# Kernel tuning notes

Measured on AMD Instinct MI355X. Metric: run time of the kernel, lower is better.

Reference implementation:

```python
import jax, jax.numpy as jnp
import numpy as np

N_HEADS = 4

def log_cosh(x):
    # numerically stable log(cosh(x)) = |x| + log1p(exp(-2|x|)) - log(2)
    ax = jnp.abs(x)
    return ax + jnp.log1p(jnp.exp(-2.0 * ax)) - jnp.log(2.0)

def setup_inputs() -> dict:
    key = jax.random.key(0)
    ks = jax.random.split(key, 7)
    B, I, A, E, H = 4, 2048, 2048, 256, N_HEADS
    return {
        "query": jax.random.normal(ks[0], (B, I, E), dtype=jnp.float32),
        "key": jax.random.normal(ks[1], (B, A, E), dtype=jnp.float32),
        "value": jax.random.normal(ks[2], (B, A, E), dtype=jnp.float32),
        "distances": jax.random.uniform(ks[3], (B, I, A), dtype=jnp.float32),
        "in_proj_w": jax.random.normal(ks[4], (3 * E, E), dtype=jnp.float32) * 0.05,
        "out_proj_w": jax.random.normal(ks[5], (E, E), dtype=jnp.float32) * 0.05,
        "mass_w": jax.random.normal(ks[6], (H, E), dtype=jnp.float32) * 0.05,
    }

def reference(query, key, value, distances, in_proj_w, out_proj_w, mass_w):
    B, I, E = query.shape
    A = key.shape[1]
    H = N_HEADS
    D = E // H
    # distance-decay additive bias: mass is (B, A, H), nonnegative via log_cosh
    mass = log_cosh(key @ mass_w.T)                       # (B, A, H)
    bias = jnp.einsum('bah,bia->bhia', -mass, distances)  # (B, H, I, A)
    # nn.MultiheadAttention (bias=False) projections
    wq, wk, wv = jnp.split(in_proj_w, 3, axis=0)          # each (E, E)
    q = (query @ wq.T).reshape(B, I, H, D).transpose(0, 2, 1, 3)  # (B,H,I,D)
    k = (key @ wk.T).reshape(B, A, H, D).transpose(0, 2, 1, 3)    # (B,H,A,D)
    v = (value @ wv.T).reshape(B, A, H, D).transpose(0, 2, 1, 3)  # (B,H,A,D)
    scale = 1.0 / jnp.sqrt(jnp.asarray(D, dtype=q.dtype))
    scores = jnp.einsum('bhid,bhad->bhia', q, k) * scale + bias
    attn = jax.nn.softmax(scores, axis=-1)
    o = jnp.einsum('bhia,bhad->bhid', attn, v)            # (B,H,I,D)
    o = o.transpose(0, 2, 1, 3).reshape(B, I, E)
    return o @ out_proj_w.T
```

## Files before the change

kernel.cpp:

```cpp
#include <hip/hip_runtime.h>
#include <hip/hip_bf16.h>
#include <math.h>

#define BB 4
#define II 2048
#define AA 2048
#define EE 256
#define HH 4

#define LOG2E 1.4426950408889634f
#define SCL   (0.125f * LOG2E)

typedef __bf16 bf16_t;
typedef bf16_t bf16x8 __attribute__((ext_vector_type(8)));
typedef bf16_t bf16x4 __attribute__((ext_vector_type(4)));
typedef float  f32x4  __attribute__((ext_vector_type(4)));

static __device__ __forceinline__ f32x4 mfma16(bf16x8 a, bf16x8 b, f32x4 c) {
    return __builtin_amdgcn_mfma_f32_16x16x32_bf16(a, b, c, 0, 0, 0);
}

static __device__ __forceinline__ void glds16(const bf16_t* g, const bf16_t* l) {
    __builtin_amdgcn_global_load_lds(
        (const __attribute__((address_space(1))) void*)g,
        (__attribute__((address_space(3))) void*)l, 16, 0, 0);
}

static __device__ __forceinline__ void proj_body(
    const float* __restrict__ Aop, const float* __restrict__ Bop,
    bf16_t* __restrict__ Cout, int m0, int n0, int TRANS, float cscale,
    bf16_t (*sA)[72], bf16_t (*sB)[72])
{
    const int t = threadIdx.x;
    const int w = t >> 6, l = t & 63, g = l >> 4, q = l & 15;
    const int wm = w >> 1, wn = w & 1;
    const int r = t >> 2, s = t & 3;

    f32x4 acc[2][2] = {};

    for (int kt = 0; kt < 4; ++kt) {
        {
            const float* ga = Aop + (size_t)(m0 + r) * EE + kt * 64 + s * 16;
            float tmp[16];
            *(f32x4*)&tmp[0]  = *(const f32x4*)(ga + 0);
            *(f32x4*)&tmp[4]  = *(const f32x4*)(ga + 4);
            *(f32x4*)&tmp[8]  = *(const f32x4*)(ga + 8);
            *(f32x4*)&tmp[12] = *(const f32x4*)(ga + 12);
            bf16x8 w0, w1;
            #pragma unroll
            for (int i = 0; i < 8; ++i) { w0[i] = (bf16_t)tmp[i]; w1[i] = (bf16_t)tmp[8 + i]; }
            *(bf16x8*)&sA[r][s * 16]     = w0;
            *(bf16x8*)&sA[r][s * 16 + 8] = w1;
        }
        {
            const float* gb = Bop + (size_t)(n0 + r) * EE + kt * 64 + s * 16;
            float tmp[16];
            *(f32x4*)&tmp[0]  = *(const f32x4*)(gb + 0);
            *(f32x4*)&tmp[4]  = *(const f32x4*)(gb + 4);
            *(f32x4*)&tmp[8]  = *(const f32x4*)(gb + 8);
            *(f32x4*)&tmp[12] = *(const f32x4*)(gb + 12);
            bf16x8 w0, w1;
            #pragma unroll
            for (int i = 0; i < 8; ++i) { w0[i] = (bf16_t)tmp[i]; w1[i] = (bf16_t)tmp[8 + i]; }
            *(bf16x8*)&sB[r][s * 16]     = w0;
            *(bf16x8*)&sB[r][s * 16 + 8] = w1;
        }
        __syncthreads();
        #pragma unroll
        for (int ks = 0; ks < 2; ++ks) {
            bf16x8 aA[2], aB[2];
            #pragma unroll
            for (int f = 0; f < 2; ++f) {
                aA[f] = *(const bf16x8*)&sA[wm * 32 + f * 16 + q][ks * 32 + g * 8];
                aB[f] = *(const bf16x8*)&sB[wn * 32 + f * 16 + q][ks * 32 + g * 8];
            }
            #pragma unroll
            for (int fm = 0; fm < 2; ++fm)
            #pragma unroll
            for (int fn = 0; fn < 2; ++fn)
                acc[fm][fn] = mfma16(aA[fm], aB[fn], acc[fm][fn]);
        }
        __syncthreads();
    }
    #pragma unroll
    for (int fm = 0; fm < 2; ++fm)
    #pragma unroll
    for (int fn = 0; fn < 2; ++fn)
    #pragma unroll
    for (int j = 0; j < 4; ++j) {
        const int m = m0 + wm * 32 + fm * 16 + g * 4 + j;
        const int n = n0 + wn * 32 + fn * 16 + q;
        const bf16_t v = (bf16_t)(acc[fm][fn][j] * cscale);
        if (TRANS == 0) {
            Cout[(size_t)m * EE + n] = v;
        } else {
            const int bb = n >> 11, a = n & (AA - 1);
            const int a6 = a & 63;
            const int p6 = (a6 & 32) | ((a6 & 12) << 1) | ((a6 & 16) >> 2) | (a6 & 3);
            Cout[(size_t)bb * (AA * EE) + (size_t)(a >> 6) * (EE * 64) + m * 64 + p6] = v;
        }
    }
}

__global__ __launch_bounds__(256) void fused_pre(
    const float* __restrict__ query, const float* __restrict__ key,
    const float* __restrict__ value, const float* __restrict__ in_w,
    const float* __restrict__ mass_w,
    bf16_t* __restrict__ Qp, bf16_t* __restrict__ Kp, bf16_t* __restrict__ Vt,
    float* __restrict__ massT)
{
    __shared__ __align__(16) bf16_t sA[64][72];
    __shared__ __align__(16) bf16_t sB[64][72];
    const int z = blockIdx.z;
    if (z == 0) {
        proj_body(query, in_w, Qp, blockIdx.x * 64, blockIdx.y * 64, 0, SCL, sA, sB);
    } else if (z == 1) {
        proj_body(key, in_w + 65536, Kp, blockIdx.x * 64, blockIdx.y * 64, 0, 1.0f, sA, sB);
    } else if (z == 2) {
        proj_body(in_w + 131072, value, Vt, blockIdx.y * 64, blockIdx.x * 64, 1, 1.0f, sA, sB);
    } else {
        const int w = threadIdx.x >> 6, l = threadIdx.x & 63;
        const int p = blockIdx.y * 128 + blockIdx.x;
        const int row0 = p * 16 + w * 4;
        f32x4 mw[HH];
        #pragma unroll
        for (int hh = 0; hh < HH; ++hh)
            mw[hh] = *(const f32x4*)(mass_w + hh * EE + l * 4);
        #pragma unroll
        for (int rr = 0; rr < 4; ++rr) {
            const int row = row0 + rr;
            f32x4 kv = *(const f32x4*)(key + (size_t)row * EE + l * 4);
            f32x4 sd;
            #pragma unroll
            for (int hh = 0; hh < HH; ++hh)
                sd[hh] = kv[0]*mw[hh][0] + kv[1]*mw[hh][1] + kv[2]*mw[hh][2] + kv[3]*mw[hh][3];
            #pragma unroll
            for (int off = 32; off >= 1; off >>= 1) {
                #pragma unroll
                for (int hh = 0; hh < HH; ++hh) sd[hh] += __shfl_xor(sd[hh], off, 64);
            }
            if (l == 0) {
                const int bb = row >> 11, a = row & (AA - 1);
                #pragma unroll
                for (int hh = 0; hh < HH; ++hh) {
                    float ax = fabsf(sd[hh]);
                    massT[((size_t)bb * HH + hh) * AA + a] =
                        (ax + log1pf(__expf(-2.0f * ax)) - 0.693147180559945f) * LOG2E;
                }
            }
        }
    }
}

__global__ __launch_bounds__(256) void out_gemm(
    const bf16_t* __restrict__ Aop, const float* __restrict__ Bop,
    float* __restrict__ Cout)
{
    __shared__ __align__(16) bf16_t sA[64][72];
    __shared__ __align__(16) bf16_t sB[64][72];
    const int t = threadIdx.x;
    const int w = t >> 6, l = t & 63, g = l >> 4, q = l & 15;
    const int wm = w >> 1, wn = w & 1;
    const int m0 = blockIdx.x * 64, n0 = blockIdx.y * 64;
    const int r = t >> 2, s = t & 3;

    f32x4 acc[2][2] = {};

    for (int kt = 0; kt < 4; ++kt) {
        {
            const bf16_t* ga = Aop + (size_t)(m0 + r) * EE + kt * 64 + s * 16;
            *(bf16x8*)&sA[r][s * 16]     = *(const bf16x8*)(ga);
            *(bf16x8*)&sA[r][s * 16 + 8] = *(const bf16x8*)(ga + 8);
        }
        {
            const float* gb = Bop + (size_t)(n0 + r) * EE + kt * 64 + s * 16;
            float tmp[16];
            *(f32x4*)&tmp[0]  = *(const f32x4*)(gb + 0);
            *(f32x4*)&tmp[4]  = *(const f32x4*)(gb + 4);
            *(f32x4*)&tmp[8]  = *(const f32x4*)(gb + 8);
            *(f32x4*)&tmp[12] = *(const f32x4*)(gb + 12);
            bf16x8 w0, w1;
            #pragma unroll
            for (int i = 0; i < 8; ++i) { w0[i] = (bf16_t)tmp[i]; w1[i] = (bf16_t)tmp[8 + i]; }
            *(bf16x8*)&sB[r][s * 16]     = w0;
            *(bf16x8*)&sB[r][s * 16 + 8] = w1;
        }
        __syncthreads();
        #pragma unroll
        for (int ks = 0; ks < 2; ++ks) {
            bf16x8 aA[2], aB[2];
            #pragma unroll
            for (int f = 0; f < 2; ++f) {
                aA[f] = *(const bf16x8*)&sA[wm * 32 + f * 16 + q][ks * 32 + g * 8];
                aB[f] = *(const bf16x8*)&sB[wn * 32 + f * 16 + q][ks * 32 + g * 8];
            }
            #pragma unroll
            for (int fm = 0; fm < 2; ++fm)
            #pragma unroll
            for (int fn = 0; fn < 2; ++fn)
                acc[fm][fn] = mfma16(aA[fm], aB[fn], acc[fm][fn]);
        }
        __syncthreads();
    }
    #pragma unroll
    for (int fm = 0; fm < 2; ++fm)
    #pragma unroll
    for (int fn = 0; fn < 2; ++fn)
    #pragma unroll
    for (int j = 0; j < 4; ++j) {
        const int m = m0 + wm * 32 + fm * 16 + g * 4 + j;
        const int n = n0 + wn * 32 + fn * 16 + q;
        Cout[(size_t)m * EE + n] = acc[fm][fn][j];
    }
}

__global__ __launch_bounds__(512, 4) void attn_kernel(
    const bf16_t* __restrict__ Qp, const bf16_t* __restrict__ Kp,
    const bf16_t* __restrict__ Vt, const float* __restrict__ massT,
    const float* __restrict__ dist, bf16_t* __restrict__ Obuf)
{
    __shared__ __align__(16) bf16_t sK[2][2][4096];
    __shared__ __align__(16) bf16_t sV[2][2][4096];
    __shared__ __align__(16) float  sM[2048];

    const int t = threadIdx.x;
    const int wv = t >> 6, l = t & 63, g = l >> 4, q = l & 15;
    const int s = wv >> 2, rg = wv & 3;
    const int h = blockIdx.y, b = blockIdx.z;
    const int i0 = blockIdx.x * 64;

    *(f32x4*)&sM[t * 4] = *(const f32x4*)(massT + ((size_t)b * HH + h) * AA + t * 4);

    bf16x8 qf[2];
    #pragma unroll
    for (int ks = 0; ks < 2; ++ks)
        qf[ks] = *(const bf16x8*)(Qp + (size_t)(b * II + i0 + rg * 16 + q) * EE
                                     + h * 64 + ks * 32 + g * 8);

    const int u0 = rg * 2;
    const int drow0 = u0 * 8 + (l >> 3);
    const int cs = (l & 7) ^ (drow0 & 7);

    const bf16_t* pkg = Kp + ((size_t)b * AA + s * 64 + drow0) * EE + h * 64 + cs * 8;
    const bf16_t* pvg = Vt + (size_t)b * (AA * EE) + (size_t)s * (EE * 64)
                           + (size_t)(h * 64 + drow0) * 64 + cs * 8;
    const float*  pdg = dist + ((size_t)b * II + i0 + rg * 16 + q) * AA + s * 64 + g * 4;

    auto stage = [&](int kb) {
        #pragma unroll
        for (int u = 0; u < 2; ++u) {
            glds16(pkg + u * (8 * EE), &sK[s][kb][(u0 + u) * 512]);
            glds16(pvg + u * (8 * 64), &sV[s][kb][(u0 + u) * 512]);
        }
    };

    f32x4 rd[4];
    auto load_dist = [&]() {
        #pragma unroll
        for (int fa = 0; fa < 4; ++fa) rd[fa] = *(const f32x4*)(pdg + fa * 16);
    };

    stage(0);
    pkg += 128 * EE; pvg += 2 * (EE * 64);
    load_dist();
    pdg += 128;
    __syncthreads();

    float mrun = -INFINITY;
    f32x4 oacc[4] = {};
    f32x4 lacc = {};
    bf16x8 vone;
    #pragma unroll
    for (int j = 0; j < 8; ++j) vone[j] = (bf16_t)1.0f;

    int ma = s * 64;

    #pragma unroll 2
    for (int k = 0; k < 16; ++k) {
        const int kb = k & 1;
        if (k < 15) {
            stage(kb ^ 1);
            pkg += 128 * EE; pvg += 2 * (EE * 64);
        }

        f32x4 st[4] = {};
        __builtin_amdgcn_s_setprio(1);
        #pragma unroll
        for (int fa = 0; fa < 4; ++fa) {
            const int row = fa * 16 + q;
            #pragma unroll
            for (int ks = 0; ks < 2; ++ks) {
                bf16x8 ak = *(const bf16x8*)&sK[s][kb][row * 64 + (((ks * 4 + g) ^ (row & 7)) * 8)];
                st[fa] = mfma16(ak, qf[ks], st[fa]);
            }
        }
        __builtin_amdgcn_s_setprio(0);

        float mloc = -INFINITY;
        #pragma unroll
        for (int fa = 0; fa < 4; ++fa) {
            f32x4 ms = *(const f32x4*)&sM[ma + fa * 16 + g * 4];
            #pragma unroll
            for (int j = 0; j < 4; ++j) {
                float sv = fmaf(-ms[j], rd[fa][j], st[fa][j]);
                st[fa][j] = sv;
                mloc = fmaxf(mloc, sv);
            }
        }
        ma += 128;
        if (k < 15) { load_dist(); pdg += 128; }

        mloc = fmaxf(mloc, __shfl_xor(mloc, 16, 64));
        mloc = fmaxf(mloc, __shfl_xor(mloc, 32, 64));
        const bool skip = __all(mloc <= mrun + 8.0f);
        float mnew = mrun;
        if (!skip) {
            mnew = fmaxf(mrun, mloc);
            const float sc = exp2f(mrun - mnew);
            mrun = mnew;
            float osc[4];
            #pragma unroll
            for (int j = 0; j < 4; ++j) osc[j] = __shfl(sc, g * 4 + j, 64);
            #pragma unroll
            for (int fd = 0; fd < 4; ++fd)
            #pragma unroll
            for (int j = 0; j < 4; ++j) oacc[fd][j] *= osc[j];
            #pragma unroll
            for (int j = 0; j < 4; ++j) lacc[j] *= osc[j];
        }

        #pragma unroll
        for (int fa = 0; fa < 4; ++fa)
        #pragma unroll
        for (int j = 0; j < 4; ++j)
            st[fa][j] = exp2f(st[fa][j] - mnew);

        bf16x8 pa[2];
        #pragma unroll
        for (int ka = 0; ka < 2; ++ka)
        #pragma unroll
        for (int j = 0; j < 8; ++j)
            pa[ka][j] = (bf16_t)st[2 * ka + (j >> 2)][j & 3];

        __builtin_amdgcn_s_setprio(1);
        #pragma unroll
        for (int ka = 0; ka < 2; ++ka) {
            #pragma unroll
            for (int fd = 0; fd < 4; ++fd) {
                const int row = fd * 16 + q;
                bf16x8 bv = *(const bf16x8*)&sV[s][kb][row * 64 + (((ka * 4 + g) ^ (row & 7)) * 8)];
                oacc[fd] = mfma16(pa[ka], bv, oacc[fd]);
            }
            lacc = mfma16(pa[ka], vone, lacc);
        }
        __builtin_amdgcn_s_setprio(0);

        __syncthreads();
    }

    float* cb = (float*)&sK[0][0][0];
    if (s == 1) {
        float* p = cb + (rg * 64 + l) * 24;
        p[0] = mrun;
        *(f32x4*)(p + 4) = lacc;
        #pragma unroll
        for (int fd = 0; fd < 4; ++fd) *(f32x4*)(p + 8 + fd * 4) = oacc[fd];
    }
    __syncthreads();
    if (s == 0) {
        const float* p = cb + (rg * 64 + l) * 24;
        const float mB = p[0];
        const f32x4 lB = *(const f32x4*)(p + 4);
        const float mS = fmaxf(mrun, mB);
        const float aS = exp2f(mrun - mS), bS = exp2f(mB - mS);
        float aSo[4], bSo[4], inv[4];
        #pragma unroll
        for (int j = 0; j < 4; ++j) {
            aSo[j] = __shfl(aS, g * 4 + j, 64);
            bSo[j] = __shfl(bS, g * 4 + j, 64);
        }
        #pragma unroll
        for (int j = 0; j < 4; ++j)
            inv[j] = 1.0f / (lacc[j] * aSo[j] + lB[j] * bSo[j]);
        #pragma unroll
        for (int fd = 0; fd < 4; ++fd) {
            f32x4 ob = *(const f32x4*)(p + 8 + fd * 4);
            #pragma unroll
            for (int j = 0; j < 4; ++j) {
                const float o = (oacc[fd][j] * aSo[j] + ob[j] * bSo[j]) * inv[j];
                Obuf[(size_t)(b * II + i0 + rg * 16 + g * 4 + j) * EE
                     + h * 64 + fd * 16 + q] = (bf16_t)o;
            }
        }
    }
}

extern "C" void kernel_launch(void* const* d_in, const int* in_sizes, int n_in,
                              void* d_out, int out_size, void* d_ws, size_t ws_size,
                              hipStream_t stream)
{
    const float* query  = (const float*)d_in[0];
    const float* key    = (const float*)d_in[1];
    const float* value  = (const float*)d_in[2];
    const float* dist   = (const float*)d_in[3];
    const float* in_w   = (const float*)d_in[4];
    const float* out_w  = (const float*)d_in[5];
    const float* mass_w = (const float*)d_in[6];
    float* out = (float*)d_out;

    char* ws = (char*)d_ws;
    bf16_t* Qp    = (bf16_t*)(ws);
    bf16_t* Kp    = (bf16_t*)(ws + 1 * 4194304);
    bf16_t* Vt    = (bf16_t*)(ws + 2 * 4194304);
    bf16_t* Obuf  = (bf16_t*)(ws + 3 * 4194304);
    float*  massT = (float*) (ws + 4 * 4194304);

    fused_pre<<<dim3(128, 4, 4), dim3(256), 0, stream>>>(
        query, key, value, in_w, mass_w, Qp, Kp, Vt, massT);
    attn_kernel<<<dim3(32, 4, 4), dim3(512), 0, stream>>>(Qp, Kp, Vt, massT, dist, Obuf);
    out_gemm<<<dim3(128, 4), dim3(256), 0, stream>>>(Obuf, out_w, out);
}
```

Before: 81.59 us.

## Restructure attention into 16-row blocks with 4-way key split reading K/V directly

The attention kernel now gives each block 16 query rows and splits the key axis four ways across waves. K, V and mass are loaded straight from global memory into registers rather than staged through LDS with barriers. The grid becomes 1D with an XCD-aware mapping so blocks sharing a batch and head land on the same XCD, improving L2 reuse. This removes LDS staging and per-iteration syncs, but adds repeated global reads of K/V across many more blocks and a 4-way merge at the end.

New measurement: 213.4 us. +161.6%, slower.

```diff
diff --git a/kernel.cpp b/kernel.cpp
--- a/kernel.cpp
+++ b/kernel.cpp
@@ -18,12 +18,6 @@
 
 static __device__ __forceinline__ f32x4 mfma16(bf16x8 a, bf16x8 b, f32x4 c) {
     return __builtin_amdgcn_mfma_f32_16x16x32_bf16(a, b, c, 0, 0, 0);
-}
-
-static __device__ __forceinline__ void glds16(const bf16_t* g, const bf16_t* l) {
-    __builtin_amdgcn_global_load_lds(
-        (const __attribute__((address_space(1))) void*)g,
-        (__attribute__((address_space(3))) void*)l, 16, 0, 0);
 }
 
 static __device__ __forceinline__ void proj_body(
@@ -214,57 +208,42 @@
     }
 }
 
-__global__ __launch_bounds__(512, 4) void attn_kernel(
+__global__ __launch_bounds__(256, 4) void attn_kernel(
     const bf16_t* __restrict__ Qp, const bf16_t* __restrict__ Kp,
     const bf16_t* __restrict__ Vt, const float* __restrict__ massT,
     const float* __restrict__ dist, bf16_t* __restrict__ Obuf)
 {
-    __shared__ __align__(16) bf16_t sK[2][2][4096];
-    __shared__ __align__(16) bf16_t sV[2][2][4096];
-    __shared__ __align__(16) float  sM[2048];
-
-    const int t = threadIdx.x;
-    const int wv = t >> 6, l = t & 63, g = l >> 4, q = l & 15;
-    const int s = wv >> 2, rg = wv & 3;
-    const int h = blockIdx.y, b = blockIdx.z;
-    const int i0 = blockIdx.x * 64;
-
-    *(f32x4*)&sM[t * 4] = *(const f32x4*)(massT + ((size_t)b * HH + h) * AA + t * 4);
+    __shared__ __align__(16) float cmb[3][64][25];
+
+    const int t0 = threadIdx.x;
+    const int w = t0 >> 6, l = t0 & 63, g = l >> 4, q = l & 15;
+
+    const int lin = blockIdx.x;
+    const int xcd = lin & 7;
+    const int r   = lin >> 3;
+    const int bh  = xcd * 2 + (r >> 7);
+    const int it  = r & 127;
+    const int b = bh >> 2, h = bh & 3;
+    const int i0 = it * 16;
 
     bf16x8 qf[2];
     #pragma unroll
     for (int ks = 0; ks < 2; ++ks)
-        qf[ks] = *(const bf16x8*)(Qp + (size_t)(b * II + i0 + rg * 16 + q) * EE
-                                     + h * 64 + ks * 32 + g * 8);
-
-    const int u0 = rg * 2;
-    const int drow0 = u0 * 8 + (l >> 3);
-    const int cs = (l & 7) ^ (drow0 & 7);
-
-    const bf16_t* pkg = Kp + ((size_t)b * AA + s * 64 + drow0) * EE + h * 64 + cs * 8;
-    const bf16_t* pvg = Vt + (size_t)b * (AA * EE) + (size_t)s * (EE * 64)
-                           + (size_t)(h * 64 + drow0) * 64 + cs * 8;
-    const float*  pdg = dist + ((size_t)b * II + i0 + rg * 16 + q) * AA + s * 64 + g * 4;
-
-    auto stage = [&](int kb) {
-        #pragma unroll
-        for (int u = 0; u < 2; ++u) {
-            glds16(pkg + u * (8 * EE), &sK[s][kb][(u0 + u) * 512]);
-            glds16(pvg + u * (8 * 64), &sV[s][kb][(u0 + u) * 512]);
-        }
-    };
-
-    f32x4 rd[4];
-    auto load_dist = [&]() {
-        #pragma unroll
-        for (int fa = 0; fa < 4; ++fa) rd[fa] = *(const f32x4*)(pdg + fa * 16);
-    };
-
-    stage(0);
-    pkg += 128 * EE; pvg += 2 * (EE * 64);
-    load_dist();
-    pdg += 128;
-    __syncthreads();
+        qf[ks] = *(const bf16x8*)(Qp + (size_t)(b * II + i0 + q) * EE + h * 64 + ks * 32 + g * 8);
+
+    const bf16_t* pK[4];
+    #pragma unroll
+    for (int fa = 0; fa < 4; ++fa)
+        pK[fa] = Kp + ((size_t)b * AA + w * 64 + fa * 16 + q) * EE + h * 64 + g * 8;
+    const bf16_t* pV = Vt + (size_t)b * (AA * EE) + (size_t)w * (EE * 64)
+                          + (h * 64 + q) * 64 + g * 8;
+    const float* pM = massT + ((size_t)b * HH + h) * AA + w * 64 + g * 4;
+    const float* pD = dist + (size_t)(b * II + i0 + q) * AA + w * 64 + g * 4;
+
+    f32x4 rd[2][4];
+    #pragma unroll
+    for (int fa = 0; fa < 4; ++fa) rd[0][fa] = *(const f32x4*)(pD + fa * 16);
+    pD += 256;
 
     float mrun = -INFINITY;
     f32x4 oacc[4] = {};
@@ -273,42 +252,54 @@
     #pragma unroll
     for (int j = 0; j < 8; ++j) vone[j] = (bf16_t)1.0f;
 
-    int ma = s * 64;
-
     #pragma unroll 2
-    for (int k = 0; k < 16; ++k) {
-        const int kb = k & 1;
-        if (k < 15) {
-            stage(kb ^ 1);
-            pkg += 128 * EE; pvg += 2 * (EE * 64);
+    for (int t = 0; t < 8; ++t) {
+        bf16x8 ak[4][2];
+        #pragma unroll
+        for (int fa = 0; fa < 4; ++fa)
+        #pragma unroll
+        for (int ks = 0; ks < 2; ++ks)
+            ak[fa][ks] = *(const bf16x8*)(pK[fa] + ks * 32);
+
+        if (t < 7) {
+            #pragma unroll
+            for (int fa = 0; fa < 4; ++fa)
+                rd[(t + 1) & 1][fa] = *(const f32x4*)(pD + fa * 16);
+            pD += 256;
         }
 
         f32x4 st[4] = {};
         __builtin_amdgcn_s_setprio(1);
         #pragma unroll
+        for (int fa = 0; fa < 4; ++fa)
+        #pragma unroll
+        for (int ks = 0; ks < 2; ++ks)
+            st[fa] = mfma16(ak[fa][ks], qf[ks], st[fa]);
+        __builtin_amdgcn_s_setprio(0);
+
+        bf16x8 vv[2][4];
+        #pragma unroll
+        for (int ka = 0; ka < 2; ++ka)
+        #pragma unroll
+        for (int fd = 0; fd < 4; ++fd)
+            vv[ka][fd] = *(const bf16x8*)(pV + fd * (16 * 64) + ka * 32);
+
+        float mloc = -INFINITY;
+        #pragma unroll
         for (int fa = 0; fa < 4; ++fa) {
-            const int row = fa * 16 + q;
-            #pragma unroll
-            for (int ks = 0; ks < 2; ++ks) {
-                bf16x8 ak = *(const bf16x8*)&sK[s][kb][row * 64 + (((ks * 4 + g) ^ (row & 7)) * 8)];
-                st[fa] = mfma16(ak, qf[ks], st[fa]);
-            }
-        }
-        __builtin_amdgcn_s_setprio(0);
-
-        float mloc = -INFINITY;
-        #pragma unroll
-        for (int fa = 0; fa < 4; ++fa) {
-            f32x4 ms = *(const f32x4*)&sM[ma + fa * 16 + g * 4];
+            f32x4 ms = *(const f32x4*)(pM + fa * 16);
             #pragma unroll
             for (int j = 0; j < 4; ++j) {
-                float sv = fmaf(-ms[j], rd[fa][j], st[fa][j]);
+                float sv = fmaf(-ms[j], rd[t & 1][fa][j], st[fa][j]);
                 st[fa][j] = sv;
                 mloc = fmaxf(mloc, sv);
             }
         }
-        ma += 128;
-        if (k < 15) { load_dist(); pdg += 128; }
+
+        #pragma unroll
+        for (int fa = 0; fa < 4; ++fa) pK[fa] += 256 * EE;
+        pV += 4 * (EE * 64);
+        pM += 256;
 
         mloc = fmaxf(mloc, __shfl_xor(mloc, 16, 64));
         mloc = fmaxf(mloc, __shfl_xor(mloc, 32, 64));
@@ -346,51 +337,54 @@
         #pragma unroll
         for (int ka = 0; ka < 2; ++ka) {
             #pragma unroll
-            for (int fd = 0; fd < 4; ++fd) {
-                const int row = fd * 16 + q;
-                bf16x8 bv = *(const bf16x8*)&sV[s][kb][row * 64 + (((ka * 4 + g) ^ (row & 7)) * 8)];
-                oacc[fd] = mfma16(pa[ka], bv, oacc[fd]);
-            }
+            for (int fd = 0; fd < 4; ++fd)
+                oacc[fd] = mfma16(pa[ka], vv[ka][fd], oacc[fd]);
             lacc = mfma16(pa[ka], vone, lacc);
         }
         __builtin_amdgcn_s_setprio(0);
-
-        __syncthreads();
-    }
-
-    float* cb = (float*)&sK[0][0][0];
-    if (s == 1) {
-        float* p = cb + (rg * 64 + l) * 24;
+    }
+
+    if (w > 0) {
+        float* p = &cmb[w - 1][l][0];
         p[0] = mrun;
         *(f32x4*)(p + 4) = lacc;
         #pragma unroll
         for (int fd = 0; fd < 4; ++fd) *(f32x4*)(p + 8 + fd * 4) = oacc[fd];
     }
     __syncthreads();
-    if (s == 0) {
-        const float* p = cb + (rg * 64 + l) * 24;
-        const float mB = p[0];
-        const f32x4 lB = *(const f32x4*)(p + 4);
-        const float mS = fmaxf(mrun, mB);
-        const float aS = exp2f(mrun - mS), bS = exp2f(mB - mS);
-        float aSo[4], bSo[4], inv[4];
+    if (w == 0) {
+        float mS = mrun;
+        float mW[3];
+        #pragma unroll
+        for (int u = 0; u < 3; ++u) { mW[u] = cmb[u][l][0]; mS = fmaxf(mS, mW[u]); }
+        const float aS0 = exp2f(mrun - mS);
+        float aSu[3];
+        #pragma unroll
+        for (int u = 0; u < 3; ++u) aSu[u] = exp2f(mW[u] - mS);
+        float s0[4], su[3][4];
         #pragma unroll
         for (int j = 0; j < 4; ++j) {
-            aSo[j] = __shfl(aS, g * 4 + j, 64);
-            bSo[j] = __shfl(bS, g * 4 + j, 64);
-        }
-        #pragma unroll
-        for (int j = 0; j < 4; ++j)
-            inv[j] = 1.0f / (lacc[j] * aSo[j] + lB[j] * bSo[j]);
-        #pragma unroll
-        for (int fd = 0; fd < 4; ++fd) {
-            f32x4 ob = *(const f32x4*)(p + 8 + fd * 4);
-            #pragma unroll
-            for (int j = 0; j < 4; ++j) {
-                const float o = (oacc[fd][j] * aSo[j] + ob[j] * bSo[j]) * inv[j];
-                Obuf[(size_t)(b * II + i0 + rg * 16 + g * 4 + j) * EE
-                     + h * 64 + fd * 16 + q] = (bf16_t)o;
-            }
+            s0[j] = __shfl(aS0, g * 4 + j, 64);
+            #pragma unroll
+            for (int u = 0; u < 3; ++u) su[u][j] = __shfl(aSu[u], g * 4 + j, 64);
+        }
+        float inv[4];
+        #pragma unroll
+        for (int j = 0; j < 4; ++j) {
+            float ls = lacc[j] * s0[j];
+            #pragma unroll
+            for (int u = 0; u < 3; ++u) ls += cmb[u][l][4 + j] * su[u][j];
+            inv[j] = 1.0f / ls;
+        }
+        #pragma unroll
+        for (int fd = 0; fd < 4; ++fd)
+        #pragma unroll
+        for (int j = 0; j < 4; ++j) {
+            float o = oacc[fd][j] * s0[j];
+            #pragma unroll
+            for (int u = 0; u < 3; ++u) o += cmb[u][l][8 + fd * 4 + j] * su[u][j];
+            Obuf[(size_t)(b * II + i0 + g * 4 + j) * EE + h * 64 + fd * 16 + q] =
+                (bf16_t)(o * inv[j]);
         }
     }
 }
@@ -417,6 +411,6 @@
 
     fused_pre<<<dim3(128, 4, 4), dim3(256), 0, stream>>>(
         query, key, value, in_w, mass_w, Qp, Kp, Vt, massT);
-    attn_kernel<<<dim3(32, 4, 4), dim3(512), 0, stream>>>(Qp, Kp, Vt, massT, dist, Obuf);
+    attn_kernel<<<dim3(2048), dim3(256), 0, stream>>>(Qp, Kp, Vt, massT, dist, Obuf);
     out_gemm<<<dim3(128, 4), dim3(256), 0, stream>>>(Obuf, out_w, out);
 }
```
